# Kernel tuning notes

Measured on AMD Instinct MI355X. Metric: run time of the kernel, lower is better.

## Reference

```python
import jax, jax.numpy as jnp
import numpy as np
import math

SPECIES = np.array([1, 6, 7, 8])
N_SPECIES = 4
HIGH_CUTOFF = 6.0
N_GAUSS = 20
ETA = 2.0
LMAX = 2
LWEIGHTS = np.ones(LMAX + 1, np.float32)
INV_FACTOR = 2.0

_comps, _w, _l = [], [], []
for _i in range(LMAX + 1):
    for _k in range(_i + 1):
        for _m in range(_i - _k + 1):
            _n = _i - _k - _m
            _comps.append((_n, _m, _k))
            _w.append(math.factorial(_i) / (math.factorial(_n) * math.factorial(_m) * math.factorial(_k)))
            _l.append(_i)
ANG_COMPS = np.array(_comps, np.int32)   # [10,3] exponents (n,m,k) for x,y,z
ANG_W = np.array(_w, np.float32)         # [10] multinomial weights
ANG_L = np.array(_l, np.int32)           # [10] angular momentum index l
PAIR_IDX = np.array([(i, j) for i in range(N_SPECIES) for j in range(i + 1, N_SPECIES)], np.int32)  # [6,2]
N_MBODY = N_SPECIES + PAIR_IDX.shape[0]  # 10
FP_SIZE = N_GAUSS * (LMAX + 1) * N_MBODY # 600


def setup_inputs() -> dict:
    key = jax.random.key(0)
    k1, k2, k3 = jax.random.split(key, 3)
    B, N = 32, 128
    coordinates = jax.random.uniform(k1, (B, N, 3), jnp.float32) * 9.0  # dense 9A box
    nuclear_charges = jnp.asarray(SPECIES, jnp.int32)[jax.random.randint(k2, (B, N), 0, N_SPECIES)]
    natom_counts = jax.random.randint(k3, (B,), 96, N + 1).astype(jnp.int32)
    return {"coordinates": coordinates, "nuclear_charges": nuclear_charges, "natom_counts": natom_counts}


def _forward(coordinates, nuclear_charges, natom_counts):
    B, N, _ = coordinates.shape
    dt = coordinates.dtype
    # dense neighbour set == all other valid atoms within cutoff (mask replaces padded pairlist)
    diff = coordinates[:, :, None, :] - coordinates[:, None, :, :]  # [B,N,M,3]
    d2 = jnp.sum(diff * diff, axis=-1)
    jvalid = jnp.arange(N)[None, None, :] < natom_counts[:, None, None]
    offdiag = ~jnp.eye(N, dtype=bool)[None]
    pair_valid = (d2 < HIGH_CUTOFF ** 2) & offdiag & jvalid
    dist = jnp.sqrt(jnp.where(pair_valid, d2, 1.0))  # safe fill for masked pairs
    maskf = pair_valid.astype(dt)

    offsets = jnp.linspace(0.0, HIGH_CUTOFF, N_GAUSS + 1, dtype=dt)[1:]  # [G]
    centered = (dist[..., None] - offsets) ** 2
    cutoffs = 0.5 * (jnp.cos(dist * (jnp.pi / HIGH_CUTOFF)) + 1.0)
    radial = jnp.sqrt(ETA / jnp.pi) * jnp.exp(-ETA * centered) * (cutoffs * maskf)[..., None]  # [B,N,M,G]

    exps = jnp.asarray(INV_FACTOR + ANG_L.astype(np.float32))  # [A], = 2 + l
    inv_scaling = jnp.power(1.0 / dist[..., None], exps) * maskf[..., None]  # [B,N,M,A]
    # integer powers x^n y^m z^k with n,m,k in {0,1,2} via power table (safe for negative bases)
    pw = jnp.stack([jnp.ones_like(diff), diff, diff * diff], axis=-1)  # [B,N,M,3(xyz),3(pow)]
    xpow, ypow, zpow = pw[:, :, :, 0, :], pw[:, :, :, 1, :], pw[:, :, :, 2, :]
    poly = xpow[..., ANG_COMPS[:, 0]] * ypow[..., ANG_COMPS[:, 1]] * zpow[..., ANG_COMPS[:, 2]]
    ang = inv_scaling * poly  # [B,N,M,A]

    # species masks: 4 single-element groups + 6 pair groups (each atom has exactly one species)
    smask = (nuclear_charges[:, :, None] == jnp.asarray(SPECIES)).astype(dt)  # [B,M,4]
    pmask = smask[..., PAIR_IDX[:, 0]] + smask[..., PAIR_IDX[:, 1]]           # [B,M,6]
    gmask = jnp.concatenate([smask, pmask], axis=-1)                          # [B,M,C=10]

    # test[c,b,n,a,g] = sum_m gmask[b,m,c] * ang[b,n,m,a] * radial[b,n,m,g]
    test = jnp.einsum('bnma,bnmg,bmc->cbnag', ang, radial, gmask)
    orb = jnp.asarray(ANG_W)[None, None, None, :, None] * test ** 2  # [C,B,N,A,G]
    seg = jax.ops.segment_sum(jnp.moveaxis(orb, 3, 0), jnp.asarray(ANG_L), num_segments=LMAX + 1)  # [L+1,C,B,N,G]
    fpg = jnp.moveaxis(seg, 0, 3)  # [C,B,N,L+1,G]

    # combination channels subtract the two single-species fingerprints
    fpp = fpg[N_SPECIES:] - fpg[PAIR_IDX[:, 0]] - fpg[PAIR_IDX[:, 1]]
    fp = jnp.moveaxis(jnp.concatenate([fpg[:N_SPECIES], fpp], axis=0), 0, 3)  # [B,N,L+1,MBODY,G]
    fp = fp * jnp.asarray(LWEIGHTS)[None, None, :, None, None]

    avalid = (jnp.arange(N)[None, :] < natom_counts[:, None]).astype(dt)
    fp = fp * avalid[:, :, None, None, None]
    return fp.reshape(B, N, FP_SIZE)


def reference(coordinates, nuclear_charges, natom_counts):
    return _forward(coordinates, nuclear_charges, natom_counts)
```

## Files before the change

### kernel.cpp

```cpp
#include <hip/hip_runtime.h>


#define NATOM 128
#define PITCH_H 232

using short8 = __attribute__((ext_vector_type(8))) short;
using f32x4  = __attribute__((ext_vector_type(4))) float;

__device__ const float d_wA[10]   = {1.f,1.f,1.f,1.f,1.f,2.f,1.f,2.f,2.f,1.f};
__device__ const int   d_abase[3] = {0, 1, 4};
__device__ const int   d_acnt[3]  = {1, 3, 6};
__device__ const int   d_PI[6]    = {0,0,0,1,1,2};
__device__ const int   d_PJ[6]    = {1,2,3,2,3,3};

__device__ __forceinline__ short pack_bf16(float x) {
    return (short)((__float_as_uint(x) + 0x8000u) >> 16);
}

__global__ __launch_bounds__(128)
void egto_kernel(const float* __restrict__ coords,
                 const int*   __restrict__ charges,
                 const int*   __restrict__ natoms,
                 float*       __restrict__ out)
{
    __shared__ __align__(16) short s_ang[10 * PITCH_H];
    __shared__ __align__(16) short s_rad[20 * PITCH_H];
    __shared__ __align__(16) float s_t[4 * 20 * 20];
    __shared__ int s_wcnt[2][4];

    const int bid  = blockIdx.x;
    const int b    = bid >> 7;
    const int n    = bid & 127;
    const int t    = threadIdx.x;
    const int wid  = t >> 6;
    const int lane = t & 63;

    const float* cb = coords + (size_t)b * NATOM * 3;
    const float cx = cb[t * 3 + 0];
    const float cy = cb[t * 3 + 1];
    const float cz = cb[t * 3 + 2];
    const float xn = cb[n * 3 + 0];
    const float yn = cb[n * 3 + 1];
    const float zn = cb[n * 3 + 2];
    const int ch = charges[b * NATOM + t];
    const int sp = (ch == 1) ? 0 : (ch == 6) ? 1 : (ch == 7) ? 2 : 3;
    const int natom = natoms[b];

    const float dx = xn - cx;
    const float dy = yn - cy;
    const float dz = zn - cz;
    const float d2 = dx * dx + dy * dy + dz * dz;
    const bool  valid = (d2 < 36.0f) && (t != n) && (t < natom);

    const unsigned long long m0 = __ballot(valid && sp == 0);
    const unsigned long long m1 = __ballot(valid && sp == 1);
    const unsigned long long m2 = __ballot(valid && sp == 2);
    const unsigned long long m3 = __ballot(valid && sp == 3);
    const unsigned long long below = (1ull << lane) - 1ull;
    const unsigned long long msel = (sp == 0) ? m0 : (sp == 1) ? m1 : (sp == 2) ? m2 : m3;
    const int rank = __popcll(msel & below);
    if (lane == 0) {
        s_wcnt[wid][0] = __popcll(m0);
        s_wcnt[wid][1] = __popcll(m1);
        s_wcnt[wid][2] = __popcll(m2);
        s_wcnt[wid][3] = __popcll(m3);
    }

    {
        uint4 z = make_uint4(0u, 0u, 0u, 0u);
        uint4* pa = reinterpret_cast<uint4*>(s_ang);
        uint4* pr = reinterpret_cast<uint4*>(s_rad);
        for (int i = t; i < 10 * PITCH_H / 8; i += 128) pa[i] = z;
        for (int i = t; i < 20 * PITCH_H / 8; i += 128) pr[i] = z;
    }
    __syncthreads();

    const int c0 = s_wcnt[0][0] + s_wcnt[1][0];
    const int c1 = s_wcnt[0][1] + s_wcnt[1][1];
    const int c2 = s_wcnt[0][2] + s_wcnt[1][2];
    const int c3 = s_wcnt[0][3] + s_wcnt[1][3];
    const int k0 = (c0 + 31) >> 5, k1 = (c1 + 31) >> 5;
    const int k2 = (c2 + 31) >> 5, k3 = (c3 + 31) >> 5;
    const int S0 = 0, S1 = k0 << 5, S2 = (k0 + k1) << 5, S3 = (k0 + k1 + k2) << 5;

    if (valid) {
        const int segb = (sp == 0) ? S0 : (sp == 1) ? S1 : (sp == 2) ? S2 : S3;
        const int slot = segb + (wid ? s_wcnt[0][sp] : 0) + rank;
        const float dist = sqrtf(d2);
        const float cutoff = 0.5f * (__cosf(dist * 0.52359877559829887f) + 1.0f);
        const float cm = 0.79788456080286536f * cutoff;
        const float invd = 1.0f / dist;
        const float i2 = invd * invd;
        const float i3 = i2 * invd;
        const float i4 = i2 * i2;
        short* ap = s_ang + slot;
        ap[0 * PITCH_H] = pack_bf16(i2);
        ap[1 * PITCH_H] = pack_bf16(i3 * dx);
        ap[2 * PITCH_H] = pack_bf16(i3 * dy);
        ap[3 * PITCH_H] = pack_bf16(i3 * dz);
        ap[4 * PITCH_H] = pack_bf16(i4 * dx * dx);
        ap[5 * PITCH_H] = pack_bf16(i4 * dx * dy);
        ap[6 * PITCH_H] = pack_bf16(i4 * dy * dy);
        ap[7 * PITCH_H] = pack_bf16(i4 * dx * dz);
        ap[8 * PITCH_H] = pack_bf16(i4 * dy * dz);
        ap[9 * PITCH_H] = pack_bf16(i4 * dz * dz);
        short* rp = s_rad + slot;
#pragma unroll
        for (int g = 0; g < 20; ++g) {
            const float dd = dist - 0.3f * (float)(g + 1);
            rp[g * PITCH_H] = pack_bf16(cm * __expf(-2.0f * dd * dd));
        }
    }
    __syncthreads();

    {
        const int q    = lane >> 4;
        const int r16  = lane & 15;
        const int aRow = (r16 < 10) ? r16 : 9;
        const int bRow = (wid * 16 + r16 < 20) ? (wid * 16 + r16) : 19;
        const short* aP = s_ang + aRow * PITCH_H + q * 8;
        const short* bP = s_rad + bRow * PITCH_H + q * 8;
        const int col = wid * 16 + r16;
        const int ks[4]   = {k0, k1, k2, k3};
        const int base[4] = {S0, S1, S2, S3};
#pragma unroll
        for (int s = 0; s < 4; ++s) {
            f32x4 acc = {0.f, 0.f, 0.f, 0.f};
            const int nk = ks[s];
            const int kb = base[s];
            for (int kk = 0; kk < nk; ++kk) {
                const short8 af = *reinterpret_cast<const short8*>(aP + kb + kk * 32);
                const short8 bf = *reinterpret_cast<const short8*>(bP + kb + kk * 32);
                acc = __builtin_amdgcn_mfma_f32_16x16x32_bf16(af, bf, acc, 0, 0, 0);
            }
            if (col < 20) {
                *reinterpret_cast<f32x4*>(&s_t[(s * 20 + col) * 20 + q * 4]) = acc;
            }
        }
    }
    __syncthreads();

    const float avalid = (n < natom) ? 1.0f : 0.0f;
    float* ob = out + (size_t)bid * 600;
    for (int o = t; o < 600; o += 128) {
        const int l   = o / 200;
        const int rem = o - 200 * l;
        const int c   = rem / 20;
        const int g   = rem - 20 * c;
        const int ab  = d_abase[l];
        const int ac  = d_acnt[l];
        float v = 0.0f;
        if (c < 4) {
            const float* tc = &s_t[(c * 20 + g) * 20];
            for (int k = 0; k < ac; ++k) {
                const int a = ab + k;
                const float tv = tc[a];
                v = fmaf(d_wA[a] * tv, tv, v);
            }
        } else {
            const int p  = c - 4;
            const float* ti = &s_t[(d_PI[p] * 20 + g) * 20];
            const float* tj = &s_t[(d_PJ[p] * 20 + g) * 20];
            for (int k = 0; k < ac; ++k) {
                const int a = ab + k;
                v = fmaf(2.0f * d_wA[a] * ti[a], tj[a], v);
            }
        }
        ob[o] = v * avalid;
    }
}

extern "C" void kernel_launch(void* const* d_in, const int* in_sizes, int n_in,
                              void* d_out, int out_size, void* d_ws, size_t ws_size,
                              hipStream_t stream) {
    (void)n_in; (void)out_size; (void)d_ws; (void)ws_size;
    const float* coords  = (const float*)d_in[0];
    const int*   charges = (const int*)d_in[1];
    const int*   natoms  = (const int*)d_in[2];
    float* out = (float*)d_out;
    const int B = in_sizes[2];
    egto_kernel<<<dim3(B * NATOM), dim3(128), 0, stream>>>(coords, charges, natoms, out);
}
```

Baseline: 76.53 us.

## Use single-wave blocks with 32x32x16 MFMA and register-resident epilogue

Switches each block from two waves to a single 64-thread wave that handles two neighbour atoms per lane. Neighbour compaction is done with wave-local ballots, so the cross-wave count exchange goes away. The contraction now uses the 32x32x16 bf16 MFMA with 16-wide species segments, which means less padding per segment. The fingerprint epilogue is computed directly from accumulator registers with one shuffle instead of going through shared memory and a final barrier. The trade-off is lower per-block parallelism and more per-thread work and registers, with correctness depending on the MFMA output lane layout mapping.

```diff
diff --git a/kernel.cpp b/kernel.cpp
--- a/kernel.cpp
+++ b/kernel.cpp
@@ -2,22 +2,16 @@
 
 
 #define NATOM 128
-#define PITCH_H 232
+#define PITCH_H 184
 
 using short8 = __attribute__((ext_vector_type(8))) short;
-using f32x4  = __attribute__((ext_vector_type(4))) float;
-
-__device__ const float d_wA[10]   = {1.f,1.f,1.f,1.f,1.f,2.f,1.f,2.f,2.f,1.f};
-__device__ const int   d_abase[3] = {0, 1, 4};
-__device__ const int   d_acnt[3]  = {1, 3, 6};
-__device__ const int   d_PI[6]    = {0,0,0,1,1,2};
-__device__ const int   d_PJ[6]    = {1,2,3,2,3,3};
+using f32x16 = __attribute__((ext_vector_type(16))) float;
 
 __device__ __forceinline__ short pack_bf16(float x) {
     return (short)((__float_as_uint(x) + 0x8000u) >> 16);
 }
 
-__global__ __launch_bounds__(128)
+__global__ __launch_bounds__(64, 4)
 void egto_kernel(const float* __restrict__ coords,
                  const int*   __restrict__ charges,
                  const int*   __restrict__ natoms,
@@ -25,70 +19,68 @@
 {
     __shared__ __align__(16) short s_ang[10 * PITCH_H];
     __shared__ __align__(16) short s_rad[20 * PITCH_H];
-    __shared__ __align__(16) float s_t[4 * 20 * 20];
-    __shared__ int s_wcnt[2][4];
 
-    const int bid  = blockIdx.x;
-    const int b    = bid >> 7;
-    const int n    = bid & 127;
-    const int t    = threadIdx.x;
-    const int wid  = t >> 6;
-    const int lane = t & 63;
+    const int bid = blockIdx.x;
+    const int b   = bid >> 7;
+    const int n   = bid & 127;
+    const int t   = threadIdx.x;
 
     const float* cb = coords + (size_t)b * NATOM * 3;
-    const float cx = cb[t * 3 + 0];
-    const float cy = cb[t * 3 + 1];
-    const float cz = cb[t * 3 + 2];
-    const float xn = cb[n * 3 + 0];
-    const float yn = cb[n * 3 + 1];
-    const float zn = cb[n * 3 + 2];
-    const int ch = charges[b * NATOM + t];
-    const int sp = (ch == 1) ? 0 : (ch == 6) ? 1 : (ch == 7) ? 2 : 3;
+    const float ax0 = cb[t * 3 + 0],        ay0 = cb[t * 3 + 1],        az0 = cb[t * 3 + 2];
+    const float ax1 = cb[(t + 64) * 3 + 0], ay1 = cb[(t + 64) * 3 + 1], az1 = cb[(t + 64) * 3 + 2];
+    const float xn  = cb[n * 3 + 0],        yn  = cb[n * 3 + 1],        zn  = cb[n * 3 + 2];
+    const int ch0 = charges[b * NATOM + t];
+    const int ch1 = charges[b * NATOM + t + 64];
     const int natom = natoms[b];
+    const int sp0 = (ch0 == 1) ? 0 : (ch0 == 6) ? 1 : (ch0 == 7) ? 2 : 3;
+    const int sp1 = (ch1 == 1) ? 0 : (ch1 == 6) ? 1 : (ch1 == 7) ? 2 : 3;
 
-    const float dx = xn - cx;
-    const float dy = yn - cy;
-    const float dz = zn - cz;
-    const float d2 = dx * dx + dy * dy + dz * dz;
-    const bool  valid = (d2 < 36.0f) && (t != n) && (t < natom);
+    const float dx0 = xn - ax0, dy0 = yn - ay0, dz0 = zn - az0;
+    const float dx1 = xn - ax1, dy1 = yn - ay1, dz1 = zn - az1;
+    const float d20 = dx0 * dx0 + dy0 * dy0 + dz0 * dz0;
+    const float d21 = dx1 * dx1 + dy1 * dy1 + dz1 * dz1;
+    const bool v0 = (d20 < 36.0f) && (t != n) && (t < natom);
+    const bool v1 = (d21 < 36.0f) && ((t + 64) != n) && ((t + 64) < natom);
 
-    const unsigned long long m0 = __ballot(valid && sp == 0);
-    const unsigned long long m1 = __ballot(valid && sp == 1);
-    const unsigned long long m2 = __ballot(valid && sp == 2);
-    const unsigned long long m3 = __ballot(valid && sp == 3);
-    const unsigned long long below = (1ull << lane) - 1ull;
-    const unsigned long long msel = (sp == 0) ? m0 : (sp == 1) ? m1 : (sp == 2) ? m2 : m3;
-    const int rank = __popcll(msel & below);
-    if (lane == 0) {
-        s_wcnt[wid][0] = __popcll(m0);
-        s_wcnt[wid][1] = __popcll(m1);
-        s_wcnt[wid][2] = __popcll(m2);
-        s_wcnt[wid][3] = __popcll(m3);
-    }
+    const unsigned long long A0 = __ballot(v0 && sp0 == 0);
+    const unsigned long long A1 = __ballot(v0 && sp0 == 1);
+    const unsigned long long A2 = __ballot(v0 && sp0 == 2);
+    const unsigned long long A3 = __ballot(v0 && sp0 == 3);
+    const unsigned long long B0 = __ballot(v1 && sp1 == 0);
+    const unsigned long long B1 = __ballot(v1 && sp1 == 1);
+    const unsigned long long B2 = __ballot(v1 && sp1 == 2);
+    const unsigned long long B3 = __ballot(v1 && sp1 == 3);
+    const int cnt0 = __popcll(A0) + __popcll(B0);
+    const int cnt1 = __popcll(A1) + __popcll(B1);
+    const int cnt2 = __popcll(A2) + __popcll(B2);
+    const int cnt3 = __popcll(A3) + __popcll(B3);
+    const int u0 = (cnt0 + 15) >> 4, u1 = (cnt1 + 15) >> 4;
+    const int u2 = (cnt2 + 15) >> 4, u3 = (cnt3 + 15) >> 4;
+    const int S0 = 0, S1 = u0 << 4, S2 = (u0 + u1) << 4, S3 = (u0 + u1 + u2) << 4;
+
+    const unsigned long long below = (1ull << t) - 1ull;
+    const unsigned long long mA0 = (sp0 == 0) ? A0 : (sp0 == 1) ? A1 : (sp0 == 2) ? A2 : A3;
+    const int seg0 = (sp0 == 0) ? S0 : (sp0 == 1) ? S1 : (sp0 == 2) ? S2 : S3;
+    const int slot0 = seg0 + __popcll(mA0 & below);
+    const unsigned long long mA1 = (sp1 == 0) ? A0 : (sp1 == 1) ? A1 : (sp1 == 2) ? A2 : A3;
+    const unsigned long long mB1 = (sp1 == 0) ? B0 : (sp1 == 1) ? B1 : (sp1 == 2) ? B2 : B3;
+    const int seg1 = (sp1 == 0) ? S0 : (sp1 == 1) ? S1 : (sp1 == 2) ? S2 : S3;
+    const int slot1 = seg1 + __popcll(mA1) + __popcll(mB1 & below);
 
     {
-        uint4 z = make_uint4(0u, 0u, 0u, 0u);
+        const uint4 z = make_uint4(0u, 0u, 0u, 0u);
         uint4* pa = reinterpret_cast<uint4*>(s_ang);
         uint4* pr = reinterpret_cast<uint4*>(s_rad);
-        for (int i = t; i < 10 * PITCH_H / 8; i += 128) pa[i] = z;
-        for (int i = t; i < 20 * PITCH_H / 8; i += 128) pr[i] = z;
+        for (int i = t; i < 230; i += 64) pa[i] = z;
+        for (int i = t; i < 460; i += 64) pr[i] = z;
     }
     __syncthreads();
 
-    const int c0 = s_wcnt[0][0] + s_wcnt[1][0];
-    const int c1 = s_wcnt[0][1] + s_wcnt[1][1];
-    const int c2 = s_wcnt[0][2] + s_wcnt[1][2];
-    const int c3 = s_wcnt[0][3] + s_wcnt[1][3];
-    const int k0 = (c0 + 31) >> 5, k1 = (c1 + 31) >> 5;
-    const int k2 = (c2 + 31) >> 5, k3 = (c3 + 31) >> 5;
-    const int S0 = 0, S1 = k0 << 5, S2 = (k0 + k1) << 5, S3 = (k0 + k1 + k2) << 5;
-
-    if (valid) {
-        const int segb = (sp == 0) ? S0 : (sp == 1) ? S1 : (sp == 2) ? S2 : S3;
-        const int slot = segb + (wid ? s_wcnt[0][sp] : 0) + rank;
+    auto emit = [&](bool v, int slot, float dx, float dy, float dz, float d2) {
+        if (!v) return;
         const float dist = sqrtf(d2);
-        const float cutoff = 0.5f * (__cosf(dist * 0.52359877559829887f) + 1.0f);
-        const float cm = 0.79788456080286536f * cutoff;
+        const float cm = 0.79788456080286536f *
+                         (0.5f * (__cosf(dist * 0.52359877559829887f) + 1.0f));
         const float invd = 1.0f / dist;
         const float i2 = invd * invd;
         const float i3 = i2 * invd;
@@ -110,64 +102,76 @@
             const float dd = dist - 0.3f * (float)(g + 1);
             rp[g * PITCH_H] = pack_bf16(cm * __expf(-2.0f * dd * dd));
         }
-    }
+    };
+    emit(v0, slot0, dx0, dy0, dz0, d20);
+    emit(v1, slot1, dx1, dy1, dz1, d21);
     __syncthreads();
 
-    {
-        const int q    = lane >> 4;
-        const int r16  = lane & 15;
-        const int aRow = (r16 < 10) ? r16 : 9;
-        const int bRow = (wid * 16 + r16 < 20) ? (wid * 16 + r16) : 19;
-        const short* aP = s_ang + aRow * PITCH_H + q * 8;
-        const short* bP = s_rad + bRow * PITCH_H + q * 8;
-        const int col = wid * 16 + r16;
-        const int ks[4]   = {k0, k1, k2, k3};
-        const int base[4] = {S0, S1, S2, S3};
+    const int r32 = t & 31;
+    const int h   = t >> 5;
+    const short* aP = s_ang + ((r32 < 10) ? r32 : 9)  * PITCH_H + h * 8;
+    const short* bP = s_rad + ((r32 < 20) ? r32 : 19) * PITCH_H + h * 8;
+    f32x16 acc[4];
+    const int Sarr[4] = {S0, S1, S2, S3};
+    const int uarr[4] = {u0, u1, u2, u3};
 #pragma unroll
-        for (int s = 0; s < 4; ++s) {
-            f32x4 acc = {0.f, 0.f, 0.f, 0.f};
-            const int nk = ks[s];
-            const int kb = base[s];
-            for (int kk = 0; kk < nk; ++kk) {
-                const short8 af = *reinterpret_cast<const short8*>(aP + kb + kk * 32);
-                const short8 bf = *reinterpret_cast<const short8*>(bP + kb + kk * 32);
-                acc = __builtin_amdgcn_mfma_f32_16x16x32_bf16(af, bf, acc, 0, 0, 0);
-            }
-            if (col < 20) {
-                *reinterpret_cast<f32x4*>(&s_t[(s * 20 + col) * 20 + q * 4]) = acc;
-            }
+    for (int s = 0; s < 4; ++s) {
+        f32x16 a = {0.f, 0.f, 0.f, 0.f, 0.f, 0.f, 0.f, 0.f,
+                    0.f, 0.f, 0.f, 0.f, 0.f, 0.f, 0.f, 0.f};
+        const int kb = Sarr[s];
+        const int nk = uarr[s];
+        for (int kk = 0; kk < nk; ++kk) {
+            const short8 af = *reinterpret_cast<const short8*>(aP + kb + kk * 16);
+            const short8 bf = *reinterpret_cast<const short8*>(bP + kb + kk * 16);
+            a = __builtin_amdgcn_mfma_f32_32x32x16_bf16(af, bf, a, 0, 0, 0);
         }
+        acc[s] = a;
     }
-    __syncthreads();
 
+    float T[4][6];
+#pragma unroll
+    for (int s = 0; s < 4; ++s)
+#pragma unroll
+        for (int r = 0; r < 6; ++r) T[s][r] = acc[s][r];
+
+    const float W0 = h ? 1.f : 0.f;
+    const float W1 = h ? 2.f : 0.f;
+    const float W2 = h ? 1.f : 0.f;
+    const float W3 = h ? 2.f : 0.f;
+    const float W4 = h ? 0.f : 2.f;
+    const float W5 = h ? 0.f : 1.f;
+    const int   src    = r32 + 32;
+    const bool  writer = (h == 0) && (r32 < 20);
     const float avalid = (n < natom) ? 1.0f : 0.0f;
-    float* ob = out + (size_t)bid * 600;
-    for (int o = t; o < 600; o += 128) {
-        const int l   = o / 200;
-        const int rem = o - 200 * l;
-        const int c   = rem / 20;
-        const int g   = rem - 20 * c;
-        const int ab  = d_abase[l];
-        const int ac  = d_acnt[l];
-        float v = 0.0f;
-        if (c < 4) {
-            const float* tc = &s_t[(c * 20 + g) * 20];
-            for (int k = 0; k < ac; ++k) {
-                const int a = ab + k;
-                const float tv = tc[a];
-                v = fmaf(d_wA[a] * tv, tv, v);
-            }
-        } else {
-            const int p  = c - 4;
-            const float* ti = &s_t[(d_PI[p] * 20 + g) * 20];
-            const float* tj = &s_t[(d_PJ[p] * 20 + g) * 20];
-            for (int k = 0; k < ac; ++k) {
-                const int a = ab + k;
-                v = fmaf(2.0f * d_wA[a] * ti[a], tj[a], v);
-            }
+    float* ob = out + (size_t)bid * 600 + r32;
+
+    auto channel = [&](const float* ti, const float* tj, float f, int c) {
+        const float pr0 = ti[0] * tj[0];
+        const float pr1 = ti[1] * tj[1];
+        const float pr2 = ti[2] * tj[2];
+        const float pr3 = ti[3] * tj[3];
+        const float pr4 = ti[4] * tj[4];
+        const float pr5 = ti[5] * tj[5];
+        const float p0 = pr0;
+        const float p1 = pr1 + pr2 + pr3;
+        float p2 = W0 * pr0 + W1 * pr1 + W2 * pr2 + W3 * pr3 + W4 * pr4 + W5 * pr5;
+        p2 += __shfl(p2, src);
+        if (writer) {
+            ob[c * 20 +   0] = f * p0 * avalid;
+            ob[c * 20 + 200] = f * p1 * avalid;
+            ob[c * 20 + 400] = f * p2 * avalid;
         }
-        ob[o] = v * avalid;
-    }
+    };
+    channel(T[0], T[0], 1.f, 0);
+    channel(T[1], T[1], 1.f, 1);
+    channel(T[2], T[2], 1.f, 2);
+    channel(T[3], T[3], 1.f, 3);
+    channel(T[0], T[1], 2.f, 4);
+    channel(T[0], T[2], 2.f, 5);
+    channel(T[0], T[3], 2.f, 6);
+    channel(T[1], T[2], 2.f, 7);
+    channel(T[1], T[3], 2.f, 8);
+    channel(T[2], T[3], 2.f, 9);
 }
 
 extern "C" void kernel_launch(void* const* d_in, const int* in_sizes, int n_in,
@@ -179,5 +183,5 @@
     const int*   natoms  = (const int*)d_in[2];
     float* out = (float*)d_out;
     const int B = in_sizes[2];
-    egto_kernel<<<dim3(B * NATOM), dim3(128), 0, stream>>>(coords, charges, natoms, out);
+    egto_kernel<<<dim3(B * NATOM), dim3(64), 0, stream>>>(coords, charges, natoms, out);
 }
```

New measurement: 67.83 us. 11.4% less time.
